# Kernel optimization log

Measured on AMD Instinct MI355X. Metric: run time of the kernel, lower is better.

The kernel has to match this reference:

```python
import jax, jax.numpy as jnp
import numpy as np

N = 512       # n_nodes (also number of per-node attention heads)
F_IN = 256    # n_feature
H = 64        # h_feature
C = 64        # n_class (must equal H for V * out broadcast)
K = 12        # top-K threshold for learned adjacency
ALPHA = 0.2   # LeakyReLU negative slope


def setup_inputs() -> dict:
    key = jax.random.key(0)
    ks = jax.random.split(key, 6)
    X = jax.random.normal(ks[0], (N, F_IN), jnp.float32)
    # stacked params of the n_nodes first-layer attention heads
    W_stack = jax.random.normal(ks[1], (N, F_IN, H), jnp.float32) * 0.05
    a_stack = jax.random.normal(ks[2], (N, 2 * H, 1), jnp.float32) * 0.05
    # output attention layer: in_Channel = h_feature * n_nodes
    W_out = jax.random.normal(ks[3], (H * N, C), jnp.float32) * 0.02
    a_out = jax.random.normal(ks[4], (2 * C, 1), jnp.float32) * 0.05
    V = jax.random.normal(ks[5], (N, H), jnp.float32) * 0.1
    return {"X": X, "W_stack": W_stack, "a_stack": a_stack,
            "W_out": W_out, "a_out": a_out, "V": V}


def gat_layer(Hx, adj, W, a):
    # Faithful to Graph_Attention_Covlayer.forward, but the O(N^2 * 2F)
    # concat tensor is algebraically collapsed: concat(Wh[i], Wh[j]) @ a
    # == (Wh @ a1)[i] + (Wh @ a2)[j], a broadcast sum.
    Wh = Hx @ W                      # (N, F)
    f = W.shape[1]
    e1 = Wh @ a[:f, 0]               # (N,)
    e2 = Wh @ a[f:, 0]               # (N,)
    S = jax.nn.leaky_relu(e1[:, None] + e2[None, :], ALPHA)  # (N, N)
    A = jax.nn.softmax(S, axis=1)    # softmax BEFORE masking, as in source
    A = jnp.where(adj > 0, A, jnp.zeros_like(A))
    out = A @ Wh                     # (N, F)
    return jax.nn.elu(out)           # concat=True -> elu


def adj_learn(V):
    A = V @ V.T                      # (N, N)
    kth = jax.lax.top_k(A.reshape(-1), K)[0][-1]
    # source: Adj = 1 where A > kth-value, else 0 (strict >)
    return jnp.where(A > kth, jnp.ones_like(A), jnp.zeros_like(A))


def reference(X, W_stack, a_stack, W_out, a_out, V):
    adj = adj_learn(V)
    # all n_nodes heads share input X and adj -> vmap over stacked params
    heads = jax.vmap(lambda W, a: gat_layer(X, adj, W, a))(W_stack, a_stack)  # (N_heads, N, H)
    # torch.cat(..., dim=1): row i = [head0_feats | head1_feats | ...]
    mid = jnp.transpose(heads, (1, 0, 2)).reshape(N, N * H)
    # dropout: eval mode -> identity
    out = gat_layer(mid, adj, W_out, a_out)  # (N, C)
    out = jax.nn.elu(V * out)
    return adj, out
```

## Files before the change

### kernel.cpp

```cpp
#include <hip/hip_runtime.h>


#define INT_OFF   0
#define CAND_OFF  128
#define KTH_OFF   3200
#define W2_OFF    3264
#define E1_OFF    134336
#define WH_OFF    142528
#define E2P_OFF   535744
#define MIDC_OFF  1584320
#define PART_OFF  535744
#define I_CNT   0
#define I_ENT   8
#define I_M     24
#define I_R     25
#define I_ROWS  32
#define I_ER    48
#define I_EJ    64
#define I_ECJ   80

__device__ __forceinline__ float leaky_(float x) { return fmaxf(x, 0.2f * x); }
__device__ __forceinline__ float elu_(float x)   { return x > 0.f ? x : __expf(x) - 1.f; }

__global__ void k1_prep(const float* __restrict__ V, float* __restrict__ wsf,
                        float* __restrict__ out) {
  int b = blockIdx.x, t = threadIdx.x;
  if (b < 512) {
    __shared__ float vi[64];
    if (t < 64) vi[t] = V[b * 64 + t];
    __syncthreads();
    #pragma unroll
    for (int jj = 0; jj < 2; ++jj) {
      int j = t + jj * 256;
      const float4* vj = reinterpret_cast<const float4*>(V + j * 64);
      float acc = 0.f;
      #pragma unroll
      for (int q = 0; q < 16; ++q) {
        float4 v4 = vj[q];
        acc += v4.x * vi[q*4] + v4.y * vi[q*4+1] + v4.z * vi[q*4+2] + v4.w * vi[q*4+3];
      }
      out[b * 512 + j] = acc;
    }
  } else {
    int base = 262144 + (b - 512) * 512 + t;
    out[base] = 0.f;
    out[base + 256] = 0.f;
    if (b == 512 && t == 0) {
      int* ip = (int*)(wsf + INT_OFF);
      ip[I_CNT] = 0;
    }
  }
}

__global__ void k2_topk_block(const float* __restrict__ A, float* __restrict__ wsf) {
  int b = blockIdx.x, l = threadIdx.x;
  const float4* src = reinterpret_cast<const float4*>(A + b * 1024);
  float v[16];
  #pragma unroll
  for (int u = 0; u < 4; ++u) {
    float4 x = src[u * 64 + l];
    v[u*4] = x.x; v[u*4+1] = x.y; v[u*4+2] = x.z; v[u*4+3] = x.w;
  }
  unsigned rm = 0;
  for (int round = 0; round < 12; ++round) {
    float m = -INFINITY; int mi = 0;
    #pragma unroll
    for (int q = 0; q < 16; ++q) {
      bool ok = ((rm >> q) & 1u) == 0u;
      if (ok && v[q] > m) { m = v[q]; mi = q; }
    }
    int idx = (l << 4) | mi;
    #pragma unroll
    for (int d = 1; d < 64; d <<= 1) {
      float ov = __shfl_xor(m, d);
      int   oi = __shfl_xor(idx, d);
      if (ov > m || (ov == m && oi < idx)) { m = ov; idx = oi; }
    }
    if (l == 0) wsf[CAND_OFF + b * 12 + round] = m;
    if ((idx >> 4) == l) rm |= 1u << (idx & 15);
  }
}

__global__ void k3_topk_final(float* __restrict__ wsf) {
  __shared__ float svw[4]; __shared__ int siw[4];
  int t = threadIdx.x, l = t & 63, w = t >> 6;
  float v[12];
  #pragma unroll
  for (int q = 0; q < 12; ++q) v[q] = wsf[CAND_OFF + t * 12 + q];
  unsigned rm = 0;
  float kth = 0.f;
  for (int round = 0; round < 12; ++round) {
    float m = -INFINITY; int mi = 0;
    #pragma unroll
    for (int q = 0; q < 12; ++q) {
      bool ok = ((rm >> q) & 1u) == 0u;
      if (ok && v[q] > m) { m = v[q]; mi = q; }
    }
    int idx = (t << 4) | mi;
    #pragma unroll
    for (int d = 1; d < 64; d <<= 1) {
      float ov = __shfl_xor(m, d);
      int   oi = __shfl_xor(idx, d);
      if (ov > m || (ov == m && oi < idx)) { m = ov; idx = oi; }
    }
    if (l == 0) { svw[w] = m; siw[w] = idx; }
    __syncthreads();
    float bm = svw[0]; int bi = siw[0];
    #pragma unroll
    for (int ww = 1; ww < 4; ++ww) {
      if (svw[ww] > bm || (svw[ww] == bm && siw[ww] < bi)) { bm = svw[ww]; bi = siw[ww]; }
    }
    if ((bi >> 4) == t) rm |= 1u << (bi & 15);
    kth = bm;
    __syncthreads();
  }
  if (t == 0) wsf[KTH_OFF] = kth;
}

__global__ void k4_adj(float* __restrict__ outAdj, float* __restrict__ wsf) {
  int b = blockIdx.x, t = threadIdx.x;
  float kth = wsf[KTH_OFF];
  int* ip = (int*)(wsf + INT_OFF);
  int base = b * 1024 + t * 4;
  float4 a = *reinterpret_cast<const float4*>(outAdj + base);
  float va[4] = { a.x, a.y, a.z, a.w };
  float ov[4];
  #pragma unroll
  for (int q = 0; q < 4; ++q) {
    bool one = va[q] > kth;
    ov[q] = one ? 1.f : 0.f;
    if (one) {
      int pos = atomicAdd(&ip[I_CNT], 1);
      if (pos < 12) ip[I_ENT + pos] = base + q;
    }
  }
  float4 o; o.x = ov[0]; o.y = ov[1]; o.z = ov[2]; o.w = ov[3];
  *reinterpret_cast<float4*>(outAdj + base) = o;
}

__global__ void k5_finalize(float* __restrict__ wsf) {
  if (threadIdx.x != 0) return;
  int* ip = (int*)(wsf + INT_OFF);
  int cnt = ip[I_CNT];
  if (cnt > 12) cnt = 12;
  if (cnt < 0)  cnt = 0;
  int e[12];
  for (int m = 0; m < cnt; ++m) e[m] = ip[I_ENT + m];
  for (int a = 1; a < cnt; ++a) {
    int key = e[a]; int b = a - 1;
    while (b >= 0 && e[b] > key) { e[b + 1] = e[b]; --b; }
    e[b + 1] = key;
  }
  int R = 0; int rows[12], er_[12], ej_[12];
  for (int m = 0; m < cnt; ++m) {
    int i2 = e[m] >> 9, j2 = e[m] & 511;
    if (R == 0 || rows[R - 1] != i2) rows[R++] = i2;
    er_[m] = R - 1; ej_[m] = j2;
  }
  ip[I_M] = cnt; ip[I_R] = R;
  for (int r = 0; r < 12; ++r) ip[I_ROWS + r] = (r < R) ? rows[r] : 0;
  for (int m = 0; m < 12; ++m) {
    ip[I_ER + m] = (m < cnt) ? er_[m] : 0;
    ip[I_EJ + m] = (m < cnt) ? ej_[m] : 0;
    int cj = -1;
    if (m < cnt) { for (int r = 0; r < R; ++r) if (rows[r] == ej_[m]) cj = r; }
    ip[I_ECJ + m] = cj;
  }
}

__global__ __launch_bounds__(256) void k6a_wpass(
    const float* __restrict__ X, const float* __restrict__ Wst,
    const float* __restrict__ ast, float* __restrict__ wsf) {
  __shared__ int   shdr[96];
  __shared__ float w1l[256], w2l[256];
  __shared__ __align__(16) float XeT[256 * 12];
  __shared__ __align__(16) float whp[4][768];
  int h = blockIdx.x, t = threadIdx.x;
  int l = t & 63, w = t >> 6;
  const int* ip = (const int*)(wsf + INT_OFF);
  if (t < 96) shdr[t] = ip[t];
  __syncthreads();
  int M = shdr[I_M], R = shdr[I_R];
  #pragma unroll
  for (int m = 0; m < 12; ++m) {
    float v = 0.f;
    if (m < M) v = X[shdr[I_EJ + m] * 256 + t];
    XeT[t * 12 + m] = v;
  }
  __syncthreads();

  const float* Wb = Wst + h * 16384;
  int fg = l >> 4, kc = (l & 15) << 2;
  float4 a1q = *reinterpret_cast<const float4*>(ast + h * 128 + kc);
  float4 a2q = *reinterpret_cast<const float4*>(ast + h * 128 + 64 + kc);
  float wh[12][4];
  #pragma unroll
  for (int m = 0; m < 12; ++m) { wh[m][0] = wh[m][1] = wh[m][2] = wh[m][3] = 0.f; }

  #pragma unroll 4
  for (int it = 0; it < 16; ++it) {
    int f = w * 64 + it * 4 + fg;
    float4 wq = *reinterpret_cast<const float4*>(Wb + f * 64 + kc);
    float p1 = wq.x*a1q.x + wq.y*a1q.y + wq.z*a1q.z + wq.w*a1q.w;
    float p2 = wq.x*a2q.x + wq.y*a2q.y + wq.z*a2q.z + wq.w*a2q.w;
    #pragma unroll
    for (int d = 1; d < 16; d <<= 1) { p1 += __shfl_xor(p1, d); p2 += __shfl_xor(p2, d); }
    if ((l & 15) == 0) { w1l[f] = p1; w2l[f] = p2; }
    const float4* xr = reinterpret_cast<const float4*>(&XeT[f * 12]);
    float4 xa = xr[0], xb = xr[1], xc = xr[2];
    float xv[12] = { xa.x, xa.y, xa.z, xa.w, xb.x, xb.y, xb.z, xb.w,
                     xc.x, xc.y, xc.z, xc.w };
    #pragma unroll
    for (int m = 0; m < 12; ++m) {
      wh[m][0] += xv[m] * wq.x;
      wh[m][1] += xv[m] * wq.y;
      wh[m][2] += xv[m] * wq.z;
      wh[m][3] += xv[m] * wq.w;
    }
  }
  #pragma unroll
  for (int m = 0; m < 12; ++m) {
    #pragma unroll
    for (int q = 0; q < 4; ++q) {
      float x = wh[m][q];
      x += __shfl_xor(x, 16);
      x += __shfl_xor(x, 32);
      wh[m][q] = x;
    }
  }
  if (l < 16) {
    #pragma unroll
    for (int m = 0; m < 12; ++m) {
      float4 vv = make_float4(wh[m][0], wh[m][1], wh[m][2], wh[m][3]);
      *reinterpret_cast<float4*>(&whp[w][m * 64 + kc]) = vv;
    }
  }
  __syncthreads();
  #pragma unroll
  for (int c = 0; c < 3; ++c) {
    int o = c * 256 + t;
    wsf[WH_OFF + h * 768 + o] = whp[0][o] + whp[1][o] + whp[2][o] + whp[3][o];
  }
  wsf[W2_OFF + h * 256 + t] = w2l[t];
  for (int r = w; r < R; r += 4) {
    int row = shdr[I_ROWS + r];
    float p = 0.f;
    #pragma unroll
    for (int s = 0; s < 4; ++s) {
      int f = s * 64 + l;
      p += X[row * 256 + f] * w1l[f];
    }
    #pragma unroll
    for (int d = 1; d < 64; d <<= 1) p += __shfl_xor(p, d);
    if (l == 0) wsf[E1_OFF + h * 16 + r] = p;
  }
}

__global__ __launch_bounds__(256) void ke2_gemm(const float* __restrict__ X,
                                                float* __restrict__ wsf) {
  __shared__ __align__(16) float As[64][68];
  __shared__ __align__(16) float Bs[64][68];
  int b = blockIdx.x, t = threadIdx.x;
  int q = b >> 6, bh = (b >> 3) & 7, bj = b & 7;
  int r = t >> 2, c0 = (t & 3) * 16;
  const float* wsrc = wsf + W2_OFF + (bh * 64 + r) * 256 + q * 64 + c0;
  const float* xsrc = X + (bj * 64 + r) * 256 + q * 64 + c0;
  #pragma unroll
  for (int u = 0; u < 4; ++u) {
    float4 a4 = *reinterpret_cast<const float4*>(wsrc + u * 4);
    float4 b4 = *reinterpret_cast<const float4*>(xsrc + u * 4);
    As[c0 + u*4 + 0][r] = a4.x; As[c0 + u*4 + 1][r] = a4.y;
    As[c0 + u*4 + 2][r] = a4.z; As[c0 + u*4 + 3][r] = a4.w;
    Bs[c0 + u*4 + 0][r] = b4.x; Bs[c0 + u*4 + 1][r] = b4.y;
    Bs[c0 + u*4 + 2][r] = b4.z; Bs[c0 + u*4 + 3][r] = b4.w;
  }
  __syncthreads();
  int th = t >> 4, tj = t & 15;
  float acc[4][4] = {};
  #pragma unroll 8
  for (int f = 0; f < 64; ++f) {
    float4 a4 = *reinterpret_cast<const float4*>(&As[f][th * 4]);
    float4 b4 = *reinterpret_cast<const float4*>(&Bs[f][tj * 4]);
    float av[4] = { a4.x, a4.y, a4.z, a4.w };
    float bv[4] = { b4.x, b4.y, b4.z, b4.w };
    #pragma unroll
    for (int i = 0; i < 4; ++i)
      #pragma unroll
      for (int j = 0; j < 4; ++j)
        acc[i][j] += av[i] * bv[j];
  }
  float* dst = wsf + E2P_OFF + q * 262144 + (bh * 64 + th * 4) * 512 + bj * 64 + tj * 4;
  #pragma unroll
  for (int i = 0; i < 4; ++i) {
    float4 o4 = make_float4(acc[i][0], acc[i][1], acc[i][2], acc[i][3]);
    *reinterpret_cast<float4*>(dst + i * 512) = o4;
  }
}

__global__ void k6c_stats(float* __restrict__ wsf) {
  __shared__ int   shdr[96];
  __shared__ float e1r[12], whl[768], e2s[512];
  __shared__ float redw[4], red4[48], mr[12], sr[12], avals[12];
  int h = blockIdx.x, t = threadIdx.x, l = t & 63, w = t >> 6;
  const int* ip = (const int*)(wsf + INT_OFF);
  if (t < 96) shdr[t] = ip[t];
  if (t >= 128 && t < 140) e1r[t - 128] = wsf[E1_OFF + h * 16 + (t - 128)];
  #pragma unroll
  for (int c = 0; c < 3; ++c) {
    int o = c * 256 + t;
    whl[o] = wsf[WH_OFF + h * 768 + o];
  }
  {
    float s0 = 0.f, s1 = 0.f;
    #pragma unroll
    for (int qq = 0; qq < 4; ++qq) {
      s0 += wsf[E2P_OFF + qq * 262144 + h * 512 + t];
      s1 += wsf[E2P_OFF + qq * 262144 + h * 512 + 256 + t];
    }
    e2s[t] = s0; e2s[t + 256] = s1;
  }
  __syncthreads();
  int M = shdr[I_M], R = shdr[I_R];
  {
    float p = fmaxf(e2s[w * 128 + l], e2s[w * 128 + 64 + l]);
    #pragma unroll
    for (int d = 1; d < 64; d <<= 1) p = fmaxf(p, __shfl_xor(p, d));
    if (l == 0) redw[w] = p;
  }
  __syncthreads();
  float maxe2 = fmaxf(fmaxf(redw[0], redw[1]), fmaxf(redw[2], redw[3]));
  for (int r = 0; r < R; ++r) {
    float e1_ = e1r[r];
    float m_ = leaky_(e1_ + maxe2);
    float pe = __expf(leaky_(e1_ + e2s[t]) - m_) + __expf(leaky_(e1_ + e2s[t + 256]) - m_);
    #pragma unroll
    for (int d = 1; d < 64; d <<= 1) pe += __shfl_xor(pe, d);
    if (l == 0) red4[r * 4 + w] = pe;
    if (t == r) mr[r] = m_;
  }
  __syncthreads();
  if (t < R) sr[t] = red4[t * 4] + red4[t * 4 + 1] + red4[t * 4 + 2] + red4[t * 4 + 3];
  __syncthreads();
  if (t < M) {
    int r = shdr[I_ER + t];
    avals[t] = __expf(leaky_(e1r[r] + e2s[shdr[I_EJ + t]]) - mr[r]) / sr[r];
  }
  __syncthreads();
  for (int r = w; r < R; r += 4) {
    float a = 0.f;
    #pragma unroll
    for (int m = 0; m < 12; ++m) {
      if (m < M && shdr[I_ER + m] == r) a += avals[m] * whl[m * 64 + l];
    }
    wsf[MIDC_OFF + r * 32768 + h * 64 + l] = elu_(a);
  }
}

__global__ void k7_wh2(const float* __restrict__ Wout, float* __restrict__ wsf) {
  __shared__ __align__(16) float midT[256 * 12];
  __shared__ float whp[4][768];
  int b = blockIdx.x, t = threadIdx.x;
  int l = t & 63, w = t >> 6;
  const int* ip = (const int*)(wsf + INT_OFF);
  int R = ip[I_R];
  #pragma unroll
  for (int m = 0; m < 12; ++m) {
    float v = 0.f;
    if (m < R) v = wsf[MIDC_OFF + m * 32768 + b * 256 + t];
    midT[t * 12 + m] = v;
  }
  __syncthreads();
  float acc[12];
  #pragma unroll
  for (int m = 0; m < 12; ++m) acc[m] = 0.f;
  #pragma unroll 2
  for (int ci = 0; ci < 64; ++ci) {
    int cc = w * 64 + ci;
    float wv = Wout[(b * 256 + cc) * 64 + l];
    const float4* xr = reinterpret_cast<const float4*>(&midT[cc * 12]);
    float4 xa = xr[0], xb = xr[1], xc = xr[2];
    acc[0] += xa.x * wv; acc[1] += xa.y * wv; acc[2]  += xa.z * wv; acc[3]  += xa.w * wv;
    acc[4] += xb.x * wv; acc[5] += xb.y * wv; acc[6]  += xb.z * wv; acc[7]  += xb.w * wv;
    acc[8] += xc.x * wv; acc[9] += xc.y * wv; acc[10] += xc.z * wv; acc[11] += xc.w * wv;
  }
  #pragma unroll
  for (int m = 0; m < 12; ++m) whp[w][m * 64 + l] = acc[m];
  __syncthreads();
  for (int o = t, c = 0; c < 3; ++c, o += 256) {
    float s = whp[0][o] + whp[1][o] + whp[2][o] + whp[3][o];
    wsf[PART_OFF + b * 768 + o] = s;
  }
}

__global__ void k8_final(const float* __restrict__ aout, const float* __restrict__ V,
                         float* __restrict__ wsf, float* __restrict__ out) {
  __shared__ float Wh2[768];
  __shared__ float e1o[12], e2o[12], mr[12], sr[12], avals[12];
  int t = threadIdx.x;
  const int* ip = (const int*)(wsf + INT_OFF);
  int M = ip[I_M], R = ip[I_R];
  for (int o = t, c = 0; c < 3; ++c, o += 256) {
    float s = 0.f;
    #pragma unroll 8
    for (int bb = 0; bb < 128; ++bb) s += wsf[PART_OFF + bb * 768 + o];
    Wh2[o] = s;
  }
  __syncthreads();
  if (t < R) {
    float s1 = 0.f, s2 = 0.f;
    for (int k = 0; k < 64; ++k) {
      float wv = Wh2[t * 64 + k];
      s1 += wv * aout[k];
      s2 += wv * aout[64 + k];
    }
    e1o[t] = s1; e2o[t] = s2;
  }
  __syncthreads();
  if (t < R) {
    float maxe = 0.f;
    for (int r = 0; r < R; ++r) maxe = fmaxf(maxe, e2o[r]);
    float m_ = leaky_(e1o[t] + maxe);
    float s = (float)(512 - R) * __expf(leaky_(e1o[t]) - m_);
    for (int r = 0; r < R; ++r) s += __expf(leaky_(e1o[t] + e2o[r]) - m_);
    mr[t] = m_; sr[t] = s;
  }
  __syncthreads();
  if (t < M) {
    int r = ip[I_ER + t];
    int cj = ip[I_ECJ + t];
    float e2v = (cj >= 0) ? e2o[cj] : 0.f;
    avals[t] = __expf(leaky_(e1o[r] + e2v) - mr[r]) / sr[r];
  }
  __syncthreads();
  int l = t & 63, w = t >> 6;
  for (int r = w; r < R; r += 4) {
    float a = 0.f;
    #pragma unroll
    for (int m = 0; m < 12; ++m) {
      if (m < M && ip[I_ER + m] == r) {
        int cj = ip[I_ECJ + m];
        float wv = (cj >= 0) ? Wh2[cj * 64 + l] : 0.f;
        a += avals[m] * wv;
      }
    }
    int row = ip[I_ROWS + r];
    float o2 = elu_(a);
    out[262144 + row * 64 + l] = elu_(V[row * 64 + l] * o2);
  }
}

extern "C" void kernel_launch(void* const* d_in, const int* in_sizes, int n_in,
                              void* d_out, int out_size, void* d_ws, size_t ws_size,
                              hipStream_t stream) {
  const float* X    = (const float*)d_in[0];
  const float* Wst  = (const float*)d_in[1];
  const float* ast  = (const float*)d_in[2];
  const float* Wout = (const float*)d_in[3];
  const float* aout = (const float*)d_in[4];
  const float* V    = (const float*)d_in[5];
  float* out = (float*)d_out;
  float* wsf = (float*)d_ws;

  k1_prep      <<<576, 256, 0, stream>>>(V, wsf, out);
  k2_topk_block<<<256,  64, 0, stream>>>(out, wsf);
  k3_topk_final<<<1,   256, 0, stream>>>(wsf);
  k4_adj       <<<256, 256, 0, stream>>>(out, wsf);
  k5_finalize  <<<1,    64, 0, stream>>>(wsf);
  k6a_wpass    <<<512, 256, 0, stream>>>(X, Wst, ast, wsf);
  ke2_gemm     <<<256, 256, 0, stream>>>(X, wsf);
  k6c_stats    <<<512, 256, 0, stream>>>(wsf);
  k7_wh2       <<<128, 256, 0, stream>>>(Wout, wsf);
  k8_final     <<<1,   256, 0, stream>>>(aout, V, wsf, out);
}
```

Baseline: 136.3 us.

## Fuse all stages into one cooperative persistent kernel with grid syncs

Replaces ten separate launches with one cooperative kernel of 512 blocks that uses grid.sync between phases. The top-K search is restructured so every block computes a per-row top-12 with (value, index) pairs, and every block then redundantly merges the candidates. This removes the atomic-based adjacency collection and the single-thread finalize kernels. The goal is to cut launch overhead and serialized tiny kernels, at the cost of grid-wide barriers, redundant per-block work, and a residency requirement of 512 blocks (launch bounds 256,4).

```diff
diff --git a/kernel.cpp b/kernel.cpp
--- a/kernel.cpp
+++ b/kernel.cpp
@@ -1,451 +1,437 @@
 #include <hip/hip_runtime.h>
-
-
-#define INT_OFF   0
-#define CAND_OFF  128
-#define KTH_OFF   3200
-#define W2_OFF    3264
-#define E1_OFF    134336
-#define WH_OFF    142528
-#define E2P_OFF   535744
-#define MIDC_OFF  1584320
-#define PART_OFF  535744
-#define I_CNT   0
-#define I_ENT   8
-#define I_M     24
-#define I_R     25
-#define I_ROWS  32
-#define I_ER    48
-#define I_EJ    64
-#define I_ECJ   80
+#include <hip/hip_cooperative_groups.h>
+
+namespace cg = cooperative_groups;
+
+
+#define CAND_OFF  0
+#define W2_OFF    12288
+#define E2P_OFF   143360
+#define PART_OFF  143360
+#define MIDC_OFF  1191936
+
+#define H_M    0
+#define H_R    1
+#define H_ROWS 2
+#define H_ER   14
+#define H_EJ   26
+#define H_ECJ  38
+
+#define S_XET  0
+#define S_WHP  3072
+#define S_W1   6144
+#define S_W2   6400
+#define S_AS   0
+#define S_BS   4352
+#define S_E2S  0
+#define S_MIDT 0
 
 __device__ __forceinline__ float leaky_(float x) { return fmaxf(x, 0.2f * x); }
 __device__ __forceinline__ float elu_(float x)   { return x > 0.f ? x : __expf(x) - 1.f; }
 
-__global__ void k1_prep(const float* __restrict__ V, float* __restrict__ wsf,
-                        float* __restrict__ out) {
-  int b = blockIdx.x, t = threadIdx.x;
-  if (b < 512) {
-    __shared__ float vi[64];
-    if (t < 64) vi[t] = V[b * 64 + t];
-    __syncthreads();
-    #pragma unroll
-    for (int jj = 0; jj < 2; ++jj) {
-      int j = t + jj * 256;
-      const float4* vj = reinterpret_cast<const float4*>(V + j * 64);
+__global__ __launch_bounds__(256, 4) void mega(
+    const float* __restrict__ X, const float* __restrict__ Wst,
+    const float* __restrict__ ast, const float* __restrict__ Wout,
+    const float* __restrict__ aout, const float* __restrict__ V,
+    float* __restrict__ wsf, float* __restrict__ out) {
+  cg::grid_group grid = cg::this_grid();
+  __shared__ __align__(16) float smem[8704];
+  __shared__ int   shdr[64];
+  __shared__ float kth_s;
+  __shared__ float e1r[12];
+  __shared__ float whl[768];
+  __shared__ float redv[4]; __shared__ int redi[4];
+  __shared__ float candv[12]; __shared__ int candi[12];
+  __shared__ int   es_s[12];
+  __shared__ float redf[48];
+  __shared__ float mr12[12], sr12[12], av12[12];
+
+  int b = blockIdx.x, t = threadIdx.x, l = t & 63, w = t >> 6;
+
+  {
+    if (t < 64) smem[t] = V[b * 64 + t];
+    __syncthreads();
+    float vr0, vr1;
+    {
+      const float4* vj = reinterpret_cast<const float4*>(V + t * 64);
       float acc = 0.f;
       #pragma unroll
       for (int q = 0; q < 16; ++q) {
         float4 v4 = vj[q];
-        acc += v4.x * vi[q*4] + v4.y * vi[q*4+1] + v4.z * vi[q*4+2] + v4.w * vi[q*4+3];
-      }
-      out[b * 512 + j] = acc;
-    }
-  } else {
-    int base = 262144 + (b - 512) * 512 + t;
-    out[base] = 0.f;
-    out[base + 256] = 0.f;
-    if (b == 512 && t == 0) {
-      int* ip = (int*)(wsf + INT_OFF);
-      ip[I_CNT] = 0;
-    }
-  }
-}
-
-__global__ void k2_topk_block(const float* __restrict__ A, float* __restrict__ wsf) {
-  int b = blockIdx.x, l = threadIdx.x;
-  const float4* src = reinterpret_cast<const float4*>(A + b * 1024);
-  float v[16];
-  #pragma unroll
-  for (int u = 0; u < 4; ++u) {
-    float4 x = src[u * 64 + l];
-    v[u*4] = x.x; v[u*4+1] = x.y; v[u*4+2] = x.z; v[u*4+3] = x.w;
-  }
-  unsigned rm = 0;
-  for (int round = 0; round < 12; ++round) {
-    float m = -INFINITY; int mi = 0;
-    #pragma unroll
-    for (int q = 0; q < 16; ++q) {
-      bool ok = ((rm >> q) & 1u) == 0u;
-      if (ok && v[q] > m) { m = v[q]; mi = q; }
-    }
-    int idx = (l << 4) | mi;
-    #pragma unroll
-    for (int d = 1; d < 64; d <<= 1) {
-      float ov = __shfl_xor(m, d);
-      int   oi = __shfl_xor(idx, d);
-      if (ov > m || (ov == m && oi < idx)) { m = ov; idx = oi; }
-    }
-    if (l == 0) wsf[CAND_OFF + b * 12 + round] = m;
-    if ((idx >> 4) == l) rm |= 1u << (idx & 15);
-  }
-}
-
-__global__ void k3_topk_final(float* __restrict__ wsf) {
-  __shared__ float svw[4]; __shared__ int siw[4];
-  int t = threadIdx.x, l = t & 63, w = t >> 6;
-  float v[12];
-  #pragma unroll
-  for (int q = 0; q < 12; ++q) v[q] = wsf[CAND_OFF + t * 12 + q];
-  unsigned rm = 0;
-  float kth = 0.f;
-  for (int round = 0; round < 12; ++round) {
-    float m = -INFINITY; int mi = 0;
-    #pragma unroll
-    for (int q = 0; q < 12; ++q) {
-      bool ok = ((rm >> q) & 1u) == 0u;
-      if (ok && v[q] > m) { m = v[q]; mi = q; }
-    }
-    int idx = (t << 4) | mi;
-    #pragma unroll
-    for (int d = 1; d < 64; d <<= 1) {
-      float ov = __shfl_xor(m, d);
-      int   oi = __shfl_xor(idx, d);
-      if (ov > m || (ov == m && oi < idx)) { m = ov; idx = oi; }
-    }
-    if (l == 0) { svw[w] = m; siw[w] = idx; }
-    __syncthreads();
-    float bm = svw[0]; int bi = siw[0];
-    #pragma unroll
-    for (int ww = 1; ww < 4; ++ww) {
-      if (svw[ww] > bm || (svw[ww] == bm && siw[ww] < bi)) { bm = svw[ww]; bi = siw[ww]; }
-    }
-    if ((bi >> 4) == t) rm |= 1u << (bi & 15);
-    kth = bm;
-    __syncthreads();
-  }
-  if (t == 0) wsf[KTH_OFF] = kth;
-}
-
-__global__ void k4_adj(float* __restrict__ outAdj, float* __restrict__ wsf) {
-  int b = blockIdx.x, t = threadIdx.x;
-  float kth = wsf[KTH_OFF];
-  int* ip = (int*)(wsf + INT_OFF);
-  int base = b * 1024 + t * 4;
-  float4 a = *reinterpret_cast<const float4*>(outAdj + base);
-  float va[4] = { a.x, a.y, a.z, a.w };
-  float ov[4];
-  #pragma unroll
-  for (int q = 0; q < 4; ++q) {
-    bool one = va[q] > kth;
-    ov[q] = one ? 1.f : 0.f;
-    if (one) {
-      int pos = atomicAdd(&ip[I_CNT], 1);
-      if (pos < 12) ip[I_ENT + pos] = base + q;
-    }
-  }
-  float4 o; o.x = ov[0]; o.y = ov[1]; o.z = ov[2]; o.w = ov[3];
-  *reinterpret_cast<float4*>(outAdj + base) = o;
-}
-
-__global__ void k5_finalize(float* __restrict__ wsf) {
-  if (threadIdx.x != 0) return;
-  int* ip = (int*)(wsf + INT_OFF);
-  int cnt = ip[I_CNT];
-  if (cnt > 12) cnt = 12;
-  if (cnt < 0)  cnt = 0;
-  int e[12];
-  for (int m = 0; m < cnt; ++m) e[m] = ip[I_ENT + m];
-  for (int a = 1; a < cnt; ++a) {
-    int key = e[a]; int b = a - 1;
-    while (b >= 0 && e[b] > key) { e[b + 1] = e[b]; --b; }
-    e[b + 1] = key;
-  }
-  int R = 0; int rows[12], er_[12], ej_[12];
-  for (int m = 0; m < cnt; ++m) {
-    int i2 = e[m] >> 9, j2 = e[m] & 511;
-    if (R == 0 || rows[R - 1] != i2) rows[R++] = i2;
-    er_[m] = R - 1; ej_[m] = j2;
-  }
-  ip[I_M] = cnt; ip[I_R] = R;
-  for (int r = 0; r < 12; ++r) ip[I_ROWS + r] = (r < R) ? rows[r] : 0;
-  for (int m = 0; m < 12; ++m) {
-    ip[I_ER + m] = (m < cnt) ? er_[m] : 0;
-    ip[I_EJ + m] = (m < cnt) ? ej_[m] : 0;
-    int cj = -1;
-    if (m < cnt) { for (int r = 0; r < R; ++r) if (rows[r] == ej_[m]) cj = r; }
-    ip[I_ECJ + m] = cj;
-  }
-}
-
-__global__ __launch_bounds__(256) void k6a_wpass(
-    const float* __restrict__ X, const float* __restrict__ Wst,
-    const float* __restrict__ ast, float* __restrict__ wsf) {
-  __shared__ int   shdr[96];
-  __shared__ float w1l[256], w2l[256];
-  __shared__ __align__(16) float XeT[256 * 12];
-  __shared__ __align__(16) float whp[4][768];
-  int h = blockIdx.x, t = threadIdx.x;
-  int l = t & 63, w = t >> 6;
-  const int* ip = (const int*)(wsf + INT_OFF);
-  if (t < 96) shdr[t] = ip[t];
-  __syncthreads();
-  int M = shdr[I_M], R = shdr[I_R];
-  #pragma unroll
-  for (int m = 0; m < 12; ++m) {
-    float v = 0.f;
-    if (m < M) v = X[shdr[I_EJ + m] * 256 + t];
-    XeT[t * 12 + m] = v;
-  }
-  __syncthreads();
-
-  const float* Wb = Wst + h * 16384;
-  int fg = l >> 4, kc = (l & 15) << 2;
-  float4 a1q = *reinterpret_cast<const float4*>(ast + h * 128 + kc);
-  float4 a2q = *reinterpret_cast<const float4*>(ast + h * 128 + 64 + kc);
-  float wh[12][4];
-  #pragma unroll
-  for (int m = 0; m < 12; ++m) { wh[m][0] = wh[m][1] = wh[m][2] = wh[m][3] = 0.f; }
-
-  #pragma unroll 4
-  for (int it = 0; it < 16; ++it) {
-    int f = w * 64 + it * 4 + fg;
-    float4 wq = *reinterpret_cast<const float4*>(Wb + f * 64 + kc);
-    float p1 = wq.x*a1q.x + wq.y*a1q.y + wq.z*a1q.z + wq.w*a1q.w;
-    float p2 = wq.x*a2q.x + wq.y*a2q.y + wq.z*a2q.z + wq.w*a2q.w;
-    #pragma unroll
-    for (int d = 1; d < 16; d <<= 1) { p1 += __shfl_xor(p1, d); p2 += __shfl_xor(p2, d); }
-    if ((l & 15) == 0) { w1l[f] = p1; w2l[f] = p2; }
-    const float4* xr = reinterpret_cast<const float4*>(&XeT[f * 12]);
-    float4 xa = xr[0], xb = xr[1], xc = xr[2];
-    float xv[12] = { xa.x, xa.y, xa.z, xa.w, xb.x, xb.y, xb.z, xb.w,
-                     xc.x, xc.y, xc.z, xc.w };
+        acc += v4.x * smem[q*4] + v4.y * smem[q*4+1] + v4.z * smem[q*4+2] + v4.w * smem[q*4+3];
+      }
+      vr0 = acc;
+    }
+    {
+      const float4* vj = reinterpret_cast<const float4*>(V + (t + 256) * 64);
+      float acc = 0.f;
+      #pragma unroll
+      for (int q = 0; q < 16; ++q) {
+        float4 v4 = vj[q];
+        acc += v4.x * smem[q*4] + v4.y * smem[q*4+1] + v4.z * smem[q*4+2] + v4.w * smem[q*4+3];
+      }
+      vr1 = acc;
+    }
+    out[b * 512 + t]       = vr0;
+    out[b * 512 + 256 + t] = vr1;
+
+    float v0 = vr0, v1 = vr1;
+    int j0 = t, j1 = t + 256;
+    for (int round = 0; round < 12; ++round) {
+      float m; int mi;
+      if (v0 >= v1) { m = v0; mi = j0; } else { m = v1; mi = j1; }
+      #pragma unroll
+      for (int d = 1; d < 64; d <<= 1) {
+        float ov = __shfl_xor(m, d);
+        int   oi = __shfl_xor(mi, d);
+        if (ov > m || (ov == m && oi < mi)) { m = ov; mi = oi; }
+      }
+      if (l == 0) { redv[w] = m; redi[w] = mi; }
+      __syncthreads();
+      float bm = redv[0]; int bi = redi[0];
+      #pragma unroll
+      for (int ww = 1; ww < 4; ++ww)
+        if (redv[ww] > bm || (redv[ww] == bm && redi[ww] < bi)) { bm = redv[ww]; bi = redi[ww]; }
+      if (t == 0) { candv[round] = bm; candi[round] = bi; }
+      if (bi == j0) v0 = -INFINITY;
+      if (bi == j1) v1 = -INFINITY;
+      __syncthreads();
+    }
+    if (t < 12) {
+      float2 c; c.x = candv[t]; c.y = __int_as_float(b * 512 + candi[t]);
+      *reinterpret_cast<float2*>(wsf + CAND_OFF + (b * 12 + t) * 2) = c;
+    }
+    if (b < 128) out[262144 + b * 256 + t] = 0.f;
+  }
+  grid.sync();
+
+  {
+    float lv[12]; int li[12];
+    #pragma unroll
+    for (int q = 0; q < 12; ++q) { lv[q] = -INFINITY; li[q] = 0x7FFFFFFF; }
+    const float2* cp = reinterpret_cast<const float2*>(wsf + CAND_OFF);
+    for (int k = 0; k < 24; ++k) {
+      float2 c = cp[t * 24 + k];
+      float cv = c.x; int ci2 = __float_as_int(c.y);
+      if (cv > lv[11] || (cv == lv[11] && ci2 < li[11])) {
+        #pragma unroll
+        for (int q = 0; q < 12; ++q) {
+          bool sw = (cv > lv[q]) || (cv == lv[q] && ci2 < li[q]);
+          if (sw) { float tv = lv[q]; int ti = li[q]; lv[q] = cv; li[q] = ci2; cv = tv; ci2 = ti; }
+        }
+      }
+    }
+    for (int round = 0; round < 12; ++round) {
+      float m = lv[0]; int mi = li[0];
+      #pragma unroll
+      for (int d = 1; d < 64; d <<= 1) {
+        float ov = __shfl_xor(m, d);
+        int   oi = __shfl_xor(mi, d);
+        if (ov > m || (ov == m && oi < mi)) { m = ov; mi = oi; }
+      }
+      if (l == 0) { redv[w] = m; redi[w] = mi; }
+      __syncthreads();
+      float bm = redv[0]; int bi = redi[0];
+      #pragma unroll
+      for (int ww = 1; ww < 4; ++ww)
+        if (redv[ww] > bm || (redv[ww] == bm && redi[ww] < bi)) { bm = redv[ww]; bi = redi[ww]; }
+      if (t == 0) { candv[round] = bm; candi[round] = bi; }
+      if (li[0] == bi) {
+        #pragma unroll
+        for (int q = 0; q < 11; ++q) { lv[q] = lv[q + 1]; li[q] = li[q + 1]; }
+        lv[11] = -INFINITY; li[11] = 0x7FFFFFFF;
+      }
+      __syncthreads();
+    }
+    if (t == 0) {
+      float kv = candv[11];
+      kth_s = kv;
+      int M = 0;
+      for (int q = 0; q < 12; ++q) {
+        if (candv[q] > kv) {
+          int ix = candi[q];
+          int p = M++;
+          while (p > 0 && es_s[p - 1] > ix) { es_s[p] = es_s[p - 1]; --p; }
+          es_s[p] = ix;
+        }
+      }
+      int R = 0;
+      for (int m2 = 0; m2 < M; ++m2) {
+        int i2 = es_s[m2] >> 9, j2 = es_s[m2] & 511;
+        if (R == 0 || shdr[H_ROWS + R - 1] != i2) { shdr[H_ROWS + R] = i2; ++R; }
+        shdr[H_ER + m2] = R - 1;
+        shdr[H_EJ + m2] = j2;
+      }
+      shdr[H_M] = M; shdr[H_R] = R;
+      for (int m2 = 0; m2 < M; ++m2) {
+        int cj = -1;
+        for (int r = 0; r < R; ++r) if (shdr[H_ROWS + r] == shdr[H_EJ + m2]) cj = r;
+        shdr[H_ECJ + m2] = cj;
+      }
+      for (int m2 = M; m2 < 12; ++m2) { shdr[H_ER + m2] = 0; shdr[H_EJ + m2] = 0; shdr[H_ECJ + m2] = -1; }
+      for (int r = R; r < 12; ++r) shdr[H_ROWS + r] = 0;
+    }
+    __syncthreads();
+  }
+
+  {
+    float kv = kth_s;
+    float a0 = out[b * 512 + t], a1 = out[b * 512 + 256 + t];
+    out[b * 512 + t]       = (a0 > kv) ? 1.f : 0.f;
+    out[b * 512 + 256 + t] = (a1 > kv) ? 1.f : 0.f;
+  }
+
+  {
+    int M = shdr[H_M], R = shdr[H_R];
     #pragma unroll
     for (int m = 0; m < 12; ++m) {
-      wh[m][0] += xv[m] * wq.x;
-      wh[m][1] += xv[m] * wq.y;
-      wh[m][2] += xv[m] * wq.z;
-      wh[m][3] += xv[m] * wq.w;
-    }
-  }
-  #pragma unroll
-  for (int m = 0; m < 12; ++m) {
-    #pragma unroll
-    for (int q = 0; q < 4; ++q) {
-      float x = wh[m][q];
-      x += __shfl_xor(x, 16);
-      x += __shfl_xor(x, 32);
-      wh[m][q] = x;
-    }
-  }
-  if (l < 16) {
+      float v = 0.f;
+      if (m < M) v = X[shdr[H_EJ + m] * 256 + t];
+      smem[S_XET + t * 12 + m] = v;
+    }
+    __syncthreads();
+
+    const float* Wb = Wst + b * 16384;
+    int fg = l >> 4, kc = (l & 15) << 2;
+    float4 a1q = *reinterpret_cast<const float4*>(ast + b * 128 + kc);
+    float4 a2q = *reinterpret_cast<const float4*>(ast + b * 128 + 64 + kc);
+    float wh[12][4];
+    #pragma unroll
+    for (int m = 0; m < 12; ++m) { wh[m][0] = wh[m][1] = wh[m][2] = wh[m][3] = 0.f; }
+
+    #pragma unroll 4
+    for (int it = 0; it < 16; ++it) {
+      int f = w * 64 + it * 4 + fg;
+      float4 wq = *reinterpret_cast<const float4*>(Wb + f * 64 + kc);
+      float p1 = wq.x*a1q.x + wq.y*a1q.y + wq.z*a1q.z + wq.w*a1q.w;
+      float p2 = wq.x*a2q.x + wq.y*a2q.y + wq.z*a2q.z + wq.w*a2q.w;
+      #pragma unroll
+      for (int d = 1; d < 16; d <<= 1) { p1 += __shfl_xor(p1, d); p2 += __shfl_xor(p2, d); }
+      if ((l & 15) == 0) { smem[S_W1 + f] = p1; smem[S_W2 + f] = p2; }
+      const float4* xr = reinterpret_cast<const float4*>(&smem[S_XET + f * 12]);
+      float4 xa = xr[0], xb = xr[1], xc = xr[2];
+      float xv[12] = { xa.x, xa.y, xa.z, xa.w, xb.x, xb.y, xb.z, xb.w,
+                       xc.x, xc.y, xc.z, xc.w };
+      #pragma unroll
+      for (int m = 0; m < 12; ++m) {
+        wh[m][0] += xv[m] * wq.x;
+        wh[m][1] += xv[m] * wq.y;
+        wh[m][2] += xv[m] * wq.z;
+        wh[m][3] += xv[m] * wq.w;
+      }
+    }
     #pragma unroll
     for (int m = 0; m < 12; ++m) {
-      float4 vv = make_float4(wh[m][0], wh[m][1], wh[m][2], wh[m][3]);
-      *reinterpret_cast<float4*>(&whp[w][m * 64 + kc]) = vv;
-    }
-  }
-  __syncthreads();
-  #pragma unroll
-  for (int c = 0; c < 3; ++c) {
-    int o = c * 256 + t;
-    wsf[WH_OFF + h * 768 + o] = whp[0][o] + whp[1][o] + whp[2][o] + whp[3][o];
-  }
-  wsf[W2_OFF + h * 256 + t] = w2l[t];
-  for (int r = w; r < R; r += 4) {
-    int row = shdr[I_ROWS + r];
-    float p = 0.f;
-    #pragma unroll
-    for (int s = 0; s < 4; ++s) {
-      int f = s * 64 + l;
-      p += X[row * 256 + f] * w1l[f];
-    }
-    #pragma unroll
-    for (int d = 1; d < 64; d <<= 1) p += __shfl_xor(p, d);
-    if (l == 0) wsf[E1_OFF + h * 16 + r] = p;
-  }
-}
-
-__global__ __launch_bounds__(256) void ke2_gemm(const float* __restrict__ X,
-                                                float* __restrict__ wsf) {
-  __shared__ __align__(16) float As[64][68];
-  __shared__ __align__(16) float Bs[64][68];
-  int b = blockIdx.x, t = threadIdx.x;
-  int q = b >> 6, bh = (b >> 3) & 7, bj = b & 7;
-  int r = t >> 2, c0 = (t & 3) * 16;
-  const float* wsrc = wsf + W2_OFF + (bh * 64 + r) * 256 + q * 64 + c0;
-  const float* xsrc = X + (bj * 64 + r) * 256 + q * 64 + c0;
-  #pragma unroll
-  for (int u = 0; u < 4; ++u) {
-    float4 a4 = *reinterpret_cast<const float4*>(wsrc + u * 4);
-    float4 b4 = *reinterpret_cast<const float4*>(xsrc + u * 4);
-    As[c0 + u*4 + 0][r] = a4.x; As[c0 + u*4 + 1][r] = a4.y;
-    As[c0 + u*4 + 2][r] = a4.z; As[c0 + u*4 + 3][r] = a4.w;
-    Bs[c0 + u*4 + 0][r] = b4.x; Bs[c0 + u*4 + 1][r] = b4.y;
-    Bs[c0 + u*4 + 2][r] = b4.z; Bs[c0 + u*4 + 3][r] = b4.w;
-  }
-  __syncthreads();
-  int th = t >> 4, tj = t & 15;
-  float acc[4][4] = {};
-  #pragma unroll 8
-  for (int f = 0; f < 64; ++f) {
-    float4 a4 = *reinterpret_cast<const float4*>(&As[f][th * 4]);
-    float4 b4 = *reinterpret_cast<const float4*>(&Bs[f][tj * 4]);
-    float av[4] = { a4.x, a4.y, a4.z, a4.w };
-    float bv[4] = { b4.x, b4.y, b4.z, b4.w };
-    #pragma unroll
-    for (int i = 0; i < 4; ++i)
-      #pragma unroll
-      for (int j = 0; j < 4; ++j)
-        acc[i][j] += av[i] * bv[j];
-  }
-  float* dst = wsf + E2P_OFF + q * 262144 + (bh * 64 + th * 4) * 512 + bj * 64 + tj * 4;
-  #pragma unroll
-  for (int i = 0; i < 4; ++i) {
-    float4 o4 = make_float4(acc[i][0], acc[i][1], acc[i][2], acc[i][3]);
-    *reinterpret_cast<float4*>(dst + i * 512) = o4;
-  }
-}
-
-__global__ void k6c_stats(float* __restrict__ wsf) {
-  __shared__ int   shdr[96];
-  __shared__ float e1r[12], whl[768], e2s[512];
-  __shared__ float redw[4], red4[48], mr[12], sr[12], avals[12];
-  int h = blockIdx.x, t = threadIdx.x, l = t & 63, w = t >> 6;
-  const int* ip = (const int*)(wsf + INT_OFF);
-  if (t < 96) shdr[t] = ip[t];
-  if (t >= 128 && t < 140) e1r[t - 128] = wsf[E1_OFF + h * 16 + (t - 128)];
-  #pragma unroll
-  for (int c = 0; c < 3; ++c) {
-    int o = c * 256 + t;
-    whl[o] = wsf[WH_OFF + h * 768 + o];
-  }
+      #pragma unroll
+      for (int q = 0; q < 4; ++q) {
+        float x = wh[m][q];
+        x += __shfl_xor(x, 16);
+        x += __shfl_xor(x, 32);
+        wh[m][q] = x;
+      }
+    }
+    if (l < 16) {
+      #pragma unroll
+      for (int m = 0; m < 12; ++m) {
+        float4 vv = make_float4(wh[m][0], wh[m][1], wh[m][2], wh[m][3]);
+        *reinterpret_cast<float4*>(&smem[S_WHP + w * 768 + m * 64 + kc]) = vv;
+      }
+    }
+    __syncthreads();
+    #pragma unroll
+    for (int c = 0; c < 3; ++c) {
+      int o = c * 256 + t;
+      whl[o] = smem[S_WHP + o] + smem[S_WHP + 768 + o] + smem[S_WHP + 1536 + o] + smem[S_WHP + 2304 + o];
+    }
+    wsf[W2_OFF + b * 256 + t] = smem[S_W2 + t];
+    for (int r = w; r < R; r += 4) {
+      int row = shdr[H_ROWS + r];
+      float p = 0.f;
+      #pragma unroll
+      for (int s = 0; s < 4; ++s) {
+        int f = s * 64 + l;
+        p += X[row * 256 + f] * smem[S_W1 + f];
+      }
+      #pragma unroll
+      for (int d = 1; d < 64; d <<= 1) p += __shfl_xor(p, d);
+      if (l == 0) e1r[r] = p;
+    }
+  }
+  grid.sync();
+
+  if (b < 256) {
+    int q = b >> 6, bh = (b >> 3) & 7, bj = b & 7;
+    int r = t >> 2, c0 = (t & 3) * 16;
+    const float* wsrc = wsf + W2_OFF + (bh * 64 + r) * 256 + q * 64 + c0;
+    const float* xsrc = X + (bj * 64 + r) * 256 + q * 64 + c0;
+    #pragma unroll
+    for (int u = 0; u < 4; ++u) {
+      float4 a4 = *reinterpret_cast<const float4*>(wsrc + u * 4);
+      float4 b4 = *reinterpret_cast<const float4*>(xsrc + u * 4);
+      smem[S_AS + (c0 + u*4 + 0) * 68 + r] = a4.x; smem[S_AS + (c0 + u*4 + 1) * 68 + r] = a4.y;
+      smem[S_AS + (c0 + u*4 + 2) * 68 + r] = a4.z; smem[S_AS + (c0 + u*4 + 3) * 68 + r] = a4.w;
+      smem[S_BS + (c0 + u*4 + 0) * 68 + r] = b4.x; smem[S_BS + (c0 + u*4 + 1) * 68 + r] = b4.y;
+      smem[S_BS + (c0 + u*4 + 2) * 68 + r] = b4.z; smem[S_BS + (c0 + u*4 + 3) * 68 + r] = b4.w;
+    }
+    __syncthreads();
+    int th = t >> 4, tj = t & 15;
+    float acc[4][4] = {};
+    #pragma unroll 8
+    for (int f = 0; f < 64; ++f) {
+      float4 a4 = *reinterpret_cast<const float4*>(&smem[S_AS + f * 68 + th * 4]);
+      float4 b4 = *reinterpret_cast<const float4*>(&smem[S_BS + f * 68 + tj * 4]);
+      float av[4] = { a4.x, a4.y, a4.z, a4.w };
+      float bv[4] = { b4.x, b4.y, b4.z, b4.w };
+      #pragma unroll
+      for (int i = 0; i < 4; ++i)
+        #pragma unroll
+        for (int j = 0; j < 4; ++j)
+          acc[i][j] += av[i] * bv[j];
+    }
+    float* dst = wsf + E2P_OFF + q * 262144 + (bh * 64 + th * 4) * 512 + bj * 64 + tj * 4;
+    #pragma unroll
+    for (int i = 0; i < 4; ++i) {
+      float4 o4 = make_float4(acc[i][0], acc[i][1], acc[i][2], acc[i][3]);
+      *reinterpret_cast<float4*>(dst + i * 512) = o4;
+    }
+  }
+  grid.sync();
+
   {
-    float s0 = 0.f, s1 = 0.f;
-    #pragma unroll
-    for (int qq = 0; qq < 4; ++qq) {
-      s0 += wsf[E2P_OFF + qq * 262144 + h * 512 + t];
-      s1 += wsf[E2P_OFF + qq * 262144 + h * 512 + 256 + t];
-    }
-    e2s[t] = s0; e2s[t + 256] = s1;
-  }
-  __syncthreads();
-  int M = shdr[I_M], R = shdr[I_R];
-  {
-    float p = fmaxf(e2s[w * 128 + l], e2s[w * 128 + 64 + l]);
-    #pragma unroll
-    for (int d = 1; d < 64; d <<= 1) p = fmaxf(p, __shfl_xor(p, d));
-    if (l == 0) redw[w] = p;
-  }
-  __syncthreads();
-  float maxe2 = fmaxf(fmaxf(redw[0], redw[1]), fmaxf(redw[2], redw[3]));
-  for (int r = 0; r < R; ++r) {
-    float e1_ = e1r[r];
-    float m_ = leaky_(e1_ + maxe2);
-    float pe = __expf(leaky_(e1_ + e2s[t]) - m_) + __expf(leaky_(e1_ + e2s[t + 256]) - m_);
-    #pragma unroll
-    for (int d = 1; d < 64; d <<= 1) pe += __shfl_xor(pe, d);
-    if (l == 0) red4[r * 4 + w] = pe;
-    if (t == r) mr[r] = m_;
-  }
-  __syncthreads();
-  if (t < R) sr[t] = red4[t * 4] + red4[t * 4 + 1] + red4[t * 4 + 2] + red4[t * 4 + 3];
-  __syncthreads();
-  if (t < M) {
-    int r = shdr[I_ER + t];
-    avals[t] = __expf(leaky_(e1r[r] + e2s[shdr[I_EJ + t]]) - mr[r]) / sr[r];
-  }
-  __syncthreads();
-  for (int r = w; r < R; r += 4) {
-    float a = 0.f;
+    int M = shdr[H_M], R = shdr[H_R];
+    {
+      float s0 = 0.f, s1 = 0.f;
+      #pragma unroll
+      for (int qq = 0; qq < 4; ++qq) {
+        s0 += wsf[E2P_OFF + qq * 262144 + b * 512 + t];
+        s1 += wsf[E2P_OFF + qq * 262144 + b * 512 + 256 + t];
+      }
+      smem[S_E2S + t] = s0; smem[S_E2S + 256 + t] = s1;
+    }
+    __syncthreads();
+    {
+      float p = fmaxf(smem[S_E2S + w * 128 + l], smem[S_E2S + w * 128 + 64 + l]);
+      #pragma unroll
+      for (int d = 1; d < 64; d <<= 1) p = fmaxf(p, __shfl_xor(p, d));
+      if (l == 0) redv[w] = p;
+    }
+    __syncthreads();
+    float maxe2 = fmaxf(fmaxf(redv[0], redv[1]), fmaxf(redv[2], redv[3]));
+    for (int r = 0; r < R; ++r) {
+      float e1_ = e1r[r];
+      float m_ = leaky_(e1_ + maxe2);
+      float pe = __expf(leaky_(e1_ + smem[S_E2S + t]) - m_) +
+                 __expf(leaky_(e1_ + smem[S_E2S + 256 + t]) - m_);
+      #pragma unroll
+      for (int d = 1; d < 64; d <<= 1) pe += __shfl_xor(pe, d);
+      if (l == 0) redf[r * 4 + w] = pe;
+      if (t == r) mr12[r] = m_;
+    }
+    __syncthreads();
+    if (t < R) sr12[t] = redf[t * 4] + redf[t * 4 + 1] + redf[t * 4 + 2] + redf[t * 4 + 3];
+    __syncthreads();
+    if (t < M) {
+      int r = shdr[H_ER + t];
+      av12[t] = __expf(leaky_(e1r[r] + smem[S_E2S + shdr[H_EJ + t]]) - mr12[r]) / sr12[r];
+    }
+    __syncthreads();
+    for (int r = w; r < R; r += 4) {
+      float a = 0.f;
+      #pragma unroll
+      for (int m = 0; m < 12; ++m) {
+        if (m < M && shdr[H_ER + m] == r) a += av12[m] * whl[m * 64 + l];
+      }
+      wsf[MIDC_OFF + r * 32768 + b * 64 + l] = elu_(a);
+    }
+  }
+  grid.sync();
+
+  if (b < 128) {
+    int R = shdr[H_R];
     #pragma unroll
     for (int m = 0; m < 12; ++m) {
-      if (m < M && shdr[I_ER + m] == r) a += avals[m] * whl[m * 64 + l];
-    }
-    wsf[MIDC_OFF + r * 32768 + h * 64 + l] = elu_(a);
-  }
-}
-
-__global__ void k7_wh2(const float* __restrict__ Wout, float* __restrict__ wsf) {
-  __shared__ __align__(16) float midT[256 * 12];
-  __shared__ float whp[4][768];
-  int b = blockIdx.x, t = threadIdx.x;
-  int l = t & 63, w = t >> 6;
-  const int* ip = (const int*)(wsf + INT_OFF);
-  int R = ip[I_R];
-  #pragma unroll
-  for (int m = 0; m < 12; ++m) {
-    float v = 0.f;
-    if (m < R) v = wsf[MIDC_OFF + m * 32768 + b * 256 + t];
-    midT[t * 12 + m] = v;
-  }
-  __syncthreads();
-  float acc[12];
-  #pragma unroll
-  for (int m = 0; m < 12; ++m) acc[m] = 0.f;
-  #pragma unroll 2
-  for (int ci = 0; ci < 64; ++ci) {
-    int cc = w * 64 + ci;
-    float wv = Wout[(b * 256 + cc) * 64 + l];
-    const float4* xr = reinterpret_cast<const float4*>(&midT[cc * 12]);
-    float4 xa = xr[0], xb = xr[1], xc = xr[2];
-    acc[0] += xa.x * wv; acc[1] += xa.y * wv; acc[2]  += xa.z * wv; acc[3]  += xa.w * wv;
-    acc[4] += xb.x * wv; acc[5] += xb.y * wv; acc[6]  += xb.z * wv; acc[7]  += xb.w * wv;
-    acc[8] += xc.x * wv; acc[9] += xc.y * wv; acc[10] += xc.z * wv; acc[11] += xc.w * wv;
-  }
-  #pragma unroll
-  for (int m = 0; m < 12; ++m) whp[w][m * 64 + l] = acc[m];
-  __syncthreads();
-  for (int o = t, c = 0; c < 3; ++c, o += 256) {
-    float s = whp[0][o] + whp[1][o] + whp[2][o] + whp[3][o];
-    wsf[PART_OFF + b * 768 + o] = s;
-  }
-}
-
-__global__ void k8_final(const float* __restrict__ aout, const float* __restrict__ V,
-                         float* __restrict__ wsf, float* __restrict__ out) {
-  __shared__ float Wh2[768];
-  __shared__ float e1o[12], e2o[12], mr[12], sr[12], avals[12];
-  int t = threadIdx.x;
-  const int* ip = (const int*)(wsf + INT_OFF);
-  int M = ip[I_M], R = ip[I_R];
-  for (int o = t, c = 0; c < 3; ++c, o += 256) {
-    float s = 0.f;
-    #pragma unroll 8
-    for (int bb = 0; bb < 128; ++bb) s += wsf[PART_OFF + bb * 768 + o];
-    Wh2[o] = s;
-  }
-  __syncthreads();
-  if (t < R) {
-    float s1 = 0.f, s2 = 0.f;
-    for (int k = 0; k < 64; ++k) {
-      float wv = Wh2[t * 64 + k];
-      s1 += wv * aout[k];
-      s2 += wv * aout[64 + k];
-    }
-    e1o[t] = s1; e2o[t] = s2;
-  }
-  __syncthreads();
-  if (t < R) {
-    float maxe = 0.f;
-    for (int r = 0; r < R; ++r) maxe = fmaxf(maxe, e2o[r]);
-    float m_ = leaky_(e1o[t] + maxe);
-    float s = (float)(512 - R) * __expf(leaky_(e1o[t]) - m_);
-    for (int r = 0; r < R; ++r) s += __expf(leaky_(e1o[t] + e2o[r]) - m_);
-    mr[t] = m_; sr[t] = s;
-  }
-  __syncthreads();
-  if (t < M) {
-    int r = ip[I_ER + t];
-    int cj = ip[I_ECJ + t];
-    float e2v = (cj >= 0) ? e2o[cj] : 0.f;
-    avals[t] = __expf(leaky_(e1o[r] + e2v) - mr[r]) / sr[r];
-  }
-  __syncthreads();
-  int l = t & 63, w = t >> 6;
-  for (int r = w; r < R; r += 4) {
-    float a = 0.f;
-    #pragma unroll
-    for (int m = 0; m < 12; ++m) {
-      if (m < M && ip[I_ER + m] == r) {
-        int cj = ip[I_ECJ + m];
-        float wv = (cj >= 0) ? Wh2[cj * 64 + l] : 0.f;
-        a += avals[m] * wv;
-      }
-    }
-    int row = ip[I_ROWS + r];
-    float o2 = elu_(a);
-    out[262144 + row * 64 + l] = elu_(V[row * 64 + l] * o2);
+      float v = 0.f;
+      if (m < R) v = wsf[MIDC_OFF + m * 32768 + b * 256 + t];
+      smem[S_MIDT + t * 12 + m] = v;
+    }
+    __syncthreads();
+    float acc[12];
+    #pragma unroll
+    for (int m = 0; m < 12; ++m) acc[m] = 0.f;
+    #pragma unroll 2
+    for (int ci = 0; ci < 64; ++ci) {
+      int cc = w * 64 + ci;
+      float wv = Wout[(b * 256 + cc) * 64 + l];
+      const float4* xr = reinterpret_cast<const float4*>(&smem[S_MIDT + cc * 12]);
+      float4 xa = xr[0], xb = xr[1], xc = xr[2];
+      acc[0] += xa.x * wv; acc[1] += xa.y * wv; acc[2]  += xa.z * wv; acc[3]  += xa.w * wv;
+      acc[4] += xb.x * wv; acc[5] += xb.y * wv; acc[6]  += xb.z * wv; acc[7]  += xb.w * wv;
+      acc[8] += xc.x * wv; acc[9] += xc.y * wv; acc[10] += xc.z * wv; acc[11] += xc.w * wv;
+    }
+    #pragma unroll
+    for (int m = 0; m < 12; ++m) smem[S_WHP + w * 768 + m * 64 + l] = acc[m];
+    __syncthreads();
+    #pragma unroll
+    for (int c = 0; c < 3; ++c) {
+      int o = c * 256 + t;
+      float s = smem[S_WHP + o] + smem[S_WHP + 768 + o] + smem[S_WHP + 1536 + o] + smem[S_WHP + 2304 + o];
+      wsf[PART_OFF + b * 768 + o] = s;
+    }
+  }
+  grid.sync();
+
+  if (b == 0) {
+    int M = shdr[H_M], R = shdr[H_R];
+    #pragma unroll
+    for (int c = 0; c < 3; ++c) {
+      int o = c * 256 + t;
+      float s = 0.f;
+      #pragma unroll 8
+      for (int bb = 0; bb < 128; ++bb) s += wsf[PART_OFF + bb * 768 + o];
+      whl[o] = s;
+    }
+    __syncthreads();
+    if (t < R) {
+      float s1 = 0.f, s2 = 0.f;
+      for (int k = 0; k < 64; ++k) {
+        float wv = whl[t * 64 + k];
+        s1 += wv * aout[k];
+        s2 += wv * aout[64 + k];
+      }
+      candv[t] = s1;
+      redf[t]  = s2;
+    }
+    __syncthreads();
+    if (t < R) {
+      float maxe = 0.f;
+      for (int r = 0; r < R; ++r) maxe = fmaxf(maxe, redf[r]);
+      float m_ = leaky_(candv[t] + maxe);
+      float s = (float)(512 - R) * __expf(leaky_(candv[t]) - m_);
+      for (int r = 0; r < R; ++r) s += __expf(leaky_(candv[t] + redf[r]) - m_);
+      mr12[t] = m_; sr12[t] = s;
+    }
+    __syncthreads();
+    if (t < M) {
+      int r  = shdr[H_ER + t];
+      int cj = shdr[H_ECJ + t];
+      float e2v = (cj >= 0) ? redf[cj] : 0.f;
+      av12[t] = __expf(leaky_(candv[r] + e2v) - mr12[r]) / sr12[r];
+    }
+    __syncthreads();
+    for (int r = w; r < R; r += 4) {
+      float a = 0.f;
+      #pragma unroll
+      for (int m = 0; m < 12; ++m) {
+        if (m < M && shdr[H_ER + m] == r) {
+          int cj = shdr[H_ECJ + m];
+          float wv = (cj >= 0) ? whl[cj * 64 + l] : 0.f;
+          a += av12[m] * wv;
+        }
+      }
+      int row = shdr[H_ROWS + r];
+      float o2 = elu_(a);
+      out[262144 + row * 64 + l] = elu_(V[row * 64 + l] * o2);
+    }
   }
 }
 
@@ -461,14 +447,8 @@
   float* out = (float*)d_out;
   float* wsf = (float*)d_ws;
 
-  k1_prep      <<<576, 256, 0, stream>>>(V, wsf, out);
-  k2_topk_block<<<256,  64, 0, stream>>>(out, wsf);
-  k3_topk_final<<<1,   256, 0, stream>>>(wsf);
-  k4_adj       <<<256, 256, 0, stream>>>(out, wsf);
-  k5_finalize  <<<1,    64, 0, stream>>>(wsf);
-  k6a_wpass    <<<512, 256, 0, stream>>>(X, Wst, ast, wsf);
-  ke2_gemm     <<<256, 256, 0, stream>>>(X, wsf);
-  k6c_stats    <<<512, 256, 0, stream>>>(wsf);
-  k7_wh2       <<<128, 256, 0, stream>>>(Wout, wsf);
-  k8_final     <<<1,   256, 0, stream>>>(aout, V, wsf, out);
+  void* args[] = { (void*)&X, (void*)&Wst, (void*)&ast, (void*)&Wout,
+                   (void*)&aout, (void*)&V, (void*)&wsf, (void*)&out };
+  hipLaunchCooperativeKernel((const void*)mega, dim3(512), dim3(256),
+                             args, 0, stream);
 }
```

Result: slower. 389.8 us (+186.1%).
